# Optimization experiments

Hardware: AMD Instinct MI355X
Metric: run time of the kernel (lower is better)

The kernel has to match this reference:

```python
import jax, jax.numpy as jnp
import numpy as np

NUM_HEADS = 8
DIM_HEAD = 64
EMBED = NUM_HEADS * DIM_HEAD  # 512
B, S, L = 2, 128, 128


def setup_inputs() -> dict:
    key = jax.random.key(0)
    k1, k2 = jax.random.split(key)
    x = jax.random.normal(k1, (B, EMBED, S, L), dtype=jnp.float32)
    # 1x1 Conv2d == pointwise linear over channels: weight [3E, E], bias [3E]
    W = jax.random.normal(k2, (3 * EMBED, EMBED), dtype=jnp.float32) * (EMBED ** -0.5)
    b = jnp.zeros((3 * EMBED,), dtype=jnp.float32)
    return {"x": x, "W": W, "b": b}


def reference(x, W, b):
    Bsz, D, S_, L_ = x.shape
    H, Dh = NUM_HEADS, DIM_HEAD
    scale = Dh ** -0.5
    # QKV projection (1x1 conv)
    qkv = jnp.einsum('oi,bisl->bosl', W, x) + b[None, :, None, None]
    q, k, v = jnp.split(qkv, 3, axis=1)
    q = q.reshape(Bsz, H, Dh, S_, L_) * scale
    k = k.reshape(Bsz, H, Dh, S_, L_)
    v = v.reshape(Bsz, H, Dh, S_, L_)
    # Column attention: attend along S axis, independently per column l
    col_scores = jnp.einsum('bhdsl,bhdtl->bhlst', q, k)      # [B,H,L,S,S]
    col_attn = jax.nn.softmax(col_scores, axis=-1)
    out_col = jnp.einsum('bhlst,bhdtl->bhdsl', col_attn, v)  # [B,H,Dh,S,L]
    # Row attention: attend along L axis, independently per row s
    row_scores = jnp.einsum('bhdsl,bhdsm->bhslm', q, k)      # [B,H,S,L,L]
    row_attn = jax.nn.softmax(row_scores, axis=-1)
    out_row = jnp.einsum('bhslm,bhdsm->bhdsl', row_attn, v)  # [B,H,Dh,S,L]
    out = (out_col + out_row).reshape(Bsz, H * Dh, S_, L_)
    return out
```

## Files before the change

kernel.cpp:

```cpp
#include <hip/hip_runtime.h>
#include <stdint.h>

#define EMB 512
#define THREE_E 1536
#define SL 16384
#define K_DIM 512

typedef unsigned short ushort;
typedef short bf16x8 __attribute__((ext_vector_type(8)));
typedef float f32x4 __attribute__((ext_vector_type(4)));

__device__ __forceinline__ ushort f2bf(float f) {
  unsigned u = __float_as_uint(f);
  u += 0x7fffu + ((u >> 16) & 1u);
  return (ushort)(u >> 16);
}
__device__ __forceinline__ float bf2f(ushort s) {
  return __uint_as_float((unsigned)s << 16);
}

__device__ __forceinline__ void async16(const ushort* g, ushort* l) {
  __builtin_amdgcn_global_load_lds(
      (const __attribute__((address_space(1))) unsigned int*)g,
      (__attribute__((address_space(3))) unsigned int*)l, 16, 0, 0);
}

__global__ __launch_bounds__(256) void wconv(const float* __restrict__ W,
                                             ushort* __restrict__ Wb) {
  int i = blockIdx.x * 256 + threadIdx.x;
  float4 f = ((const float4*)W)[i];
  uint2 o;
  o.x = (unsigned)f2bf(f.x) | ((unsigned)f2bf(f.y) << 16);
  o.y = (unsigned)f2bf(f.z) | ((unsigned)f2bf(f.w) << 16);
  ((uint2*)Wb)[i] = o;
}

__global__ __launch_bounds__(256) void xpose(const float* __restrict__ x,
                                             ushort* __restrict__ xT) {
  __shared__ ushort t[64][65];
  int b = blockIdx.z;
  int i0 = blockIdx.y * 64;
  int n0 = blockIdx.x * 64;
  int c = threadIdx.x & 63;
  int r0 = threadIdx.x >> 6;
  const float* xp = x + ((size_t)(b * EMB + i0)) * SL + n0;
  #pragma unroll
  for (int rr = 0; rr < 16; rr++) {
    int r = r0 * 16 + rr;
    t[r][c] = f2bf(xp[(size_t)r * SL + c]);
  }
  __syncthreads();
  ushort* op = xT + ((size_t)(b * SL + n0)) * EMB + i0;
  #pragma unroll
  for (int rr = 0; rr < 16; rr++) {
    int rn = r0 * 16 + rr;
    op[(size_t)rn * EMB + c] = t[c][rn];
  }
}

__global__ __launch_bounds__(256) void qkv_gemm(const ushort* __restrict__ Wb,
                                                const ushort* __restrict__ xT,
                                                const float* __restrict__ bias,
                                                ushort* __restrict__ rowQ) {
  __shared__ __align__(16) char sm[34816];
  ushort* As = (ushort*)sm;
  ushort* Bs = (ushort*)(sm + 16384);
  const int tid = threadIdx.x;
  const int b = blockIdx.z;
  const int m0 = blockIdx.y * 128;
  const int n0 = blockIdx.x * 128;
  const int lane = tid & 63;
  const int w = tid >> 6;
  const int wr = (w >> 1) * 64;
  const int wc = (w & 1) * 64;
  const int l15 = lane & 15;
  const int quad = lane >> 4;
  const ushort* xb = xT + (size_t)b * SL * EMB;
  f32x4 acc[4][4] = {};
  const int r8 = lane >> 3;
  const int cg = (lane & 7) ^ r8;
  for (int k0 = 0; k0 < K_DIM; k0 += 64) {
    __syncthreads();
    #pragma unroll
    for (int t = 0; t < 4; t++) {
      int seg = 4 * w + t;
      int row = seg * 8 + r8;
      async16(&Wb[(size_t)(m0 + row) * K_DIM + k0 + cg * 8], &As[seg * 512]);
      async16(&xb[(size_t)(n0 + row) * K_DIM + k0 + cg * 8], &Bs[seg * 512]);
    }
    __syncthreads();
    #pragma unroll
    for (int ks = 0; ks < 2; ks++) {
      bf16x8 av[4], bv[4];
      #pragma unroll
      for (int mt = 0; mt < 4; mt++) {
        int row = wr + mt * 16 + l15;
        av[mt] = *(const bf16x8*)&As[row * 64 + (((ks * 4 + quad) ^ (row & 7)) * 8)];
      }
      #pragma unroll
      for (int nt = 0; nt < 4; nt++) {
        int row = wc + nt * 16 + l15;
        bv[nt] = *(const bf16x8*)&Bs[row * 64 + (((ks * 4 + quad) ^ (row & 7)) * 8)];
      }
      #pragma unroll
      for (int mt = 0; mt < 4; mt++)
        #pragma unroll
        for (int nt = 0; nt < 4; nt++)
          acc[mt][nt] = __builtin_amdgcn_mfma_f32_16x16x32_bf16(av[mt], bv[nt], acc[mt][nt], 0, 0, 0);
    }
  }
  __syncthreads();
  {
    ushort* epi = (ushort*)sm;
    const float sc = (m0 < EMB) ? 0.125f : 1.0f;
    const int q4r = quad * 4;
    #pragma unroll
    for (int mt = 0; mt < 4; mt++) {
      int mb = wr + mt * 16 + q4r;
      float b0 = bias[m0 + mb], b1 = bias[m0 + mb + 1];
      float b2 = bias[m0 + mb + 2], b3 = bias[m0 + mb + 3];
      #pragma unroll
      for (int nt = 0; nt < 4; nt++) {
        int l = wc + nt * 16 + l15;
        unsigned u0 = f2bf((acc[mt][nt][0] + b0) * sc);
        unsigned u1 = f2bf((acc[mt][nt][1] + b1) * sc);
        unsigned u2 = f2bf((acc[mt][nt][2] + b2) * sc);
        unsigned u3 = f2bf((acc[mt][nt][3] + b3) * sc);
        uint2 pk;
        pk.x = u0 | (u1 << 16);
        pk.y = u2 | (u3 << 16);
        *(uint2*)&epi[l * 136 + mb] = pk;
      }
    }
  }
  __syncthreads();
  {
    const ushort* epi = (const ushort*)sm;
    const int sel = m0 >> 9;
    const int hb = (m0 & 511) >> 6;
    const int s = blockIdx.x;
    #pragma unroll
    for (int it = 0; it < 8; it++) {
      int flat = it * 2048 + tid * 8;
      int head = flat >> 13;
      int rem = flat & 8191;
      int l = rem >> 6;
      int dd = rem & 63;
      size_t dst = ((((size_t)(b * 3 + sel) * 8 + hb + head) * 128 + s) * 128 + l) * 64 + dd;
      *(uint4*)&rowQ[dst] = *(const uint4*)&epi[l * 136 + head * 64 + dd];
    }
  }
}

template <int COL>
__global__ __launch_bounds__(256) void attn3(const ushort* __restrict__ qkv,
                                             ushort* __restrict__ tmp,
                                             float* __restrict__ out) {
  __shared__ ushort Ks[128 * 64];
  __shared__ ushort Vt[64 * 136];
  __shared__ ushort Ps[64 * 136];
  const int tid = threadIdx.x;
  const int fixed = blockIdx.x;
  const int h = blockIdx.y, b = blockIdx.z;
  const int w = tid >> 6, lane = tid & 63, l15 = lane & 15, quad = lane >> 4;
  const size_t off = COL ? (size_t)fixed * 64 : (size_t)fixed * 8192;
  const size_t tstr = COL ? 8192 : 64;
  const ushort* Qg = qkv + ((size_t)(b * 3 + 0) * 8 + h) * 1048576 + off;
  const ushort* Kg = Qg + (size_t)8 * 1048576;
  const ushort* Vg = Qg + (size_t)16 * 1048576;
  ushort* tb = tmp + (size_t)(b * 8 + h) * 1048576;
  {
    int r8k = lane >> 3;
    int cgk = (lane & 7) ^ r8k;
    #pragma unroll
    for (int t = 0; t < 4; t++) {
      int seg = 4 * w + t;
      int row = seg * 8 + r8k;
      async16(&Kg[(size_t)row * tstr + cgk * 8], &Ks[seg * 512]);
    }
  }
  {
    int trow = tid >> 3, d0 = (tid & 7) * 8, dg = tid & 7;
    #pragma unroll
    for (int it = 0; it < 4; it++) {
      int t = trow + it * 32;
      uint4 vv = *(const uint4*)&Vg[(size_t)t * tstr + d0];
      ushort* vs = (ushort*)&vv;
      #pragma unroll
      for (int k = 0; k < 8; k++) {
        int i = (k + dg) & 7;
        Vt[(d0 + i) * 136 + t] = vs[i];
      }
    }
  }
  bf16x8 aq[2][2];
  #pragma unroll
  for (int c = 0; c < 2; c++) {
    const ushort* qp = Qg + (size_t)(c * 64 + w * 16 + l15) * tstr + quad * 8;
    aq[c][0] = *(const bf16x8*)qp;
    aq[c][1] = *(const bf16x8*)(qp + 32);
  }
  uint2 treg[2][4];
  if (!COL) {
    #pragma unroll
    for (int c = 0; c < 2; c++) {
      const ushort* tp = tb + (size_t)(c * 64 + w * 16 + l15) * 8192 + (size_t)fixed * 64 + quad * 4;
      #pragma unroll
      for (int mt = 0; mt < 4; mt++) treg[c][mt] = *(const uint2*)(tp + mt * 16);
    }
  }
  __syncthreads();
  const int rx = l15 & 7;
  #pragma unroll
  for (int c = 0; c < 2; c++) {
    f32x4 accS[8];
    #pragma unroll
    for (int nt = 0; nt < 8; nt++) {
      int row = nt * 16 + l15;
      bf16x8 bk0 = *(const bf16x8*)&Ks[row * 64 + ((quad ^ rx) * 8)];
      bf16x8 bk1 = *(const bf16x8*)&Ks[row * 64 + (((quad + 4) ^ rx) * 8)];
      f32x4 z = {0.f, 0.f, 0.f, 0.f};
      z = __builtin_amdgcn_mfma_f32_16x16x32_bf16(aq[c][0], bk0, z, 0, 0, 0);
      z = __builtin_amdgcn_mfma_f32_16x16x32_bf16(aq[c][1], bk1, z, 0, 0, 0);
      accS[nt] = z;
    }
    float inv[4];
    #pragma unroll
    for (int r = 0; r < 4; r++) {
      float mx = accS[0][r];
      #pragma unroll
      for (int nt = 1; nt < 8; nt++) mx = fmaxf(mx, accS[nt][r]);
      mx = fmaxf(mx, __shfl_xor(mx, 1));
      mx = fmaxf(mx, __shfl_xor(mx, 2));
      mx = fmaxf(mx, __shfl_xor(mx, 4));
      mx = fmaxf(mx, __shfl_xor(mx, 8));
      float s = 0.f;
      #pragma unroll
      for (int nt = 0; nt < 8; nt++) {
        float p = __builtin_amdgcn_exp2f((accS[nt][r] - mx) * 1.44269504088896f);
        accS[nt][r] = p;
        s += p;
      }
      s += __shfl_xor(s, 1);
      s += __shfl_xor(s, 2);
      s += __shfl_xor(s, 4);
      s += __shfl_xor(s, 8);
      inv[r] = 1.0f / s;
    }
    asm volatile("s_waitcnt lgkmcnt(0)" ::: "memory");
    #pragma unroll
    for (int nt = 0; nt < 8; nt++)
      #pragma unroll
      for (int r = 0; r < 4; r++)
        Ps[(w * 16 + quad * 4 + r) * 136 + nt * 16 + l15] = f2bf(accS[nt][r] * inv[r]);
    asm volatile("s_waitcnt lgkmcnt(0)" ::: "memory");
    f32x4 accO[4] = {{0.f,0.f,0.f,0.f},{0.f,0.f,0.f,0.f},{0.f,0.f,0.f,0.f},{0.f,0.f,0.f,0.f}};
    #pragma unroll
    for (int kf = 0; kf < 4; kf++) {
      bf16x8 p = *(const bf16x8*)&Ps[(w * 16 + l15) * 136 + kf * 32 + quad * 8];
      #pragma unroll
      for (int t4 = 0; t4 < 4; t4++) {
        bf16x8 v = *(const bf16x8*)&Vt[(t4 * 16 + l15) * 136 + kf * 32 + quad * 8];
        accO[t4] = COL ? __builtin_amdgcn_mfma_f32_16x16x32_bf16(p, v, accO[t4], 0, 0, 0)
                       : __builtin_amdgcn_mfma_f32_16x16x32_bf16(v, p, accO[t4], 0, 0, 0);
      }
    }
    if (COL) {
      ushort* tp = tb + (size_t)fixed * 8192 + c * 4096;
      #pragma unroll
      for (int t4 = 0; t4 < 4; t4++)
        #pragma unroll
        for (int r = 0; r < 4; r++)
          tp[(w * 16 + quad * 4 + r) * 64 + t4 * 16 + l15] = f2bf(accO[t4][r]);
    } else {
      float* ob = out + (size_t)(b * EMB + h * 64) * SL + (size_t)fixed * 128 + c * 64 + w * 16 + l15;
      #pragma unroll
      for (int t4 = 0; t4 < 4; t4++) {
        const ushort* tr = (const ushort*)&treg[c][t4];
        #pragma unroll
        for (int r = 0; r < 4; r++)
          ob[(size_t)(t4 * 16 + quad * 4 + r) * SL] = accO[t4][r] + bf2f(tr[r]);
      }
    }
  }
}

extern "C" void kernel_launch(void* const* d_in, const int* in_sizes, int n_in,
                              void* d_out, int out_size, void* d_ws, size_t ws_size,
                              hipStream_t stream) {
  const float* x = (const float*)d_in[0];
  const float* W = (const float*)d_in[1];
  const float* bias = (const float*)d_in[2];
  float* out = (float*)d_out;
  ushort* rowQ = (ushort*)d_ws;
  ushort* xT = (ushort*)((char*)d_ws + 100663296);
  ushort* tmp = (ushort*)((char*)d_ws + 100663296);
  ushort* Wb = (ushort*)((char*)d_ws + 134217728);

  hipLaunchKernelGGL(wconv, dim3(768), dim3(256), 0, stream, W, Wb);
  hipLaunchKernelGGL(xpose, dim3(256, 8, 2), dim3(256), 0, stream, x, xT);
  hipLaunchKernelGGL(qkv_gemm, dim3(128, 12, 2), dim3(256), 0, stream, Wb, xT, bias, rowQ);
  hipLaunchKernelGGL(attn3<1>, dim3(128, 8, 2), dim3(256), 0, stream, rowQ, tmp, out);
  hipLaunchKernelGGL(attn3<0>, dim3(128, 8, 2), dim3(256), 0, stream, rowQ, tmp, out);
}
```

Before: 259.5 us.

## Rewrite QKV GEMM as 256x256 tiles with double-buffered async LDS pipeline

The QKV projection GEMM moves from 128x128 tiles with 4 waves and a single LDS buffer to 256x256 tiles with 8 waves and double-buffered 128KB shared memory. Global-to-LDS async loads for the next K slice are interleaved with MFMA phases using explicit vmcnt/lgkmcnt waits, barriers and s_setprio. The aim is to hide load latency and raise arithmetic intensity per block. The epilogue now stages per-wave tiles to write the row-layout output. The cost is much larger LDS use, fewer blocks (768 instead of 3072) and fragile hand-tuned synchronisation.

```diff
diff --git a/kernel.cpp b/kernel.cpp
--- a/kernel.cpp
+++ b/kernel.cpp
@@ -58,98 +58,154 @@
   }
 }
 
-__global__ __launch_bounds__(256) void qkv_gemm(const ushort* __restrict__ Wb,
-                                                const ushort* __restrict__ xT,
-                                                const float* __restrict__ bias,
-                                                ushort* __restrict__ rowQ) {
-  __shared__ __align__(16) char sm[34816];
-  ushort* As = (ushort*)sm;
-  ushort* Bs = (ushort*)(sm + 16384);
+__global__ __launch_bounds__(512, 2) void qkv_gemm(const ushort* __restrict__ Wb,
+                                                   const ushort* __restrict__ xT,
+                                                   const float* __restrict__ bias,
+                                                   ushort* __restrict__ rowQ) {
+  __shared__ __align__(16) char sm[131072];
+  ushort* const A0 = (ushort*)sm;
+  ushort* const B0 = (ushort*)(sm + 32768);
+  ushort* const A1 = (ushort*)(sm + 65536);
+  ushort* const B1 = (ushort*)(sm + 98304);
   const int tid = threadIdx.x;
-  const int b = blockIdx.z;
-  const int m0 = blockIdx.y * 128;
-  const int n0 = blockIdx.x * 128;
-  const int lane = tid & 63;
-  const int w = tid >> 6;
-  const int wr = (w >> 1) * 64;
-  const int wc = (w & 1) * 64;
-  const int l15 = lane & 15;
-  const int quad = lane >> 4;
-  const ushort* xb = xT + (size_t)b * SL * EMB;
-  f32x4 acc[4][4] = {};
+  const int bz = blockIdx.z;
+  const int m0 = blockIdx.y * 256;
+  const int n0 = blockIdx.x * 256;
+  const int lane = tid & 63, w = tid >> 6;
+  const int wm = w >> 2, wn = w & 3;
+  const int l15 = lane & 15, quad = lane >> 4;
   const int r8 = lane >> 3;
-  const int cg = (lane & 7) ^ r8;
-  for (int k0 = 0; k0 < K_DIM; k0 += 64) {
-    __syncthreads();
-    #pragma unroll
-    for (int t = 0; t < 4; t++) {
-      int seg = 4 * w + t;
-      int row = seg * 8 + r8;
-      async16(&Wb[(size_t)(m0 + row) * K_DIM + k0 + cg * 8], &As[seg * 512]);
-      async16(&xb[(size_t)(n0 + row) * K_DIM + k0 + cg * 8], &Bs[seg * 512]);
-    }
-    __syncthreads();
-    #pragma unroll
-    for (int ks = 0; ks < 2; ks++) {
-      bf16x8 av[4], bv[4];
-      #pragma unroll
-      for (int mt = 0; mt < 4; mt++) {
-        int row = wr + mt * 16 + l15;
-        av[mt] = *(const bf16x8*)&As[row * 64 + (((ks * 4 + quad) ^ (row & 7)) * 8)];
-      }
-      #pragma unroll
-      for (int nt = 0; nt < 4; nt++) {
-        int row = wc + nt * 16 + l15;
-        bv[nt] = *(const bf16x8*)&Bs[row * 64 + (((ks * 4 + quad) ^ (row & 7)) * 8)];
-      }
-      #pragma unroll
-      for (int mt = 0; mt < 4; mt++)
-        #pragma unroll
-        for (int nt = 0; nt < 4; nt++)
-          acc[mt][nt] = __builtin_amdgcn_mfma_f32_16x16x32_bf16(av[mt], bv[nt], acc[mt][nt], 0, 0, 0);
-    }
-  }
+  const int cg8 = ((lane & 7) ^ r8) * 8;
+  const int rx = l15 & 7;
+  const ushort* Wt = Wb + (size_t)m0 * K_DIM;
+  const ushort* Xt = xT + ((size_t)bz * SL + n0) * K_DIM;
+
+  f32x4 acc[8][4] = {};
+  bf16x8 av[4][2], bv0[2][2], bv1[2][2];
+
+#define STG(gb, lb)                                                       \
+  async16((gb) + (size_t)(w * 8 + r8) * K_DIM + cg8, (lb) + w * 512);     \
+  async16((gb) + (size_t)(w * 8 + r8 + 64) * K_DIM + cg8, (lb) + w * 512 + 4096)
+
+#define LDA(AP, MH)                                                           \
+  _Pragma("unroll") for (int mt = 0; mt < 4; mt++) {                          \
+    const int row = wm * 128 + (MH) * 64 + mt * 16 + l15;                     \
+    av[mt][0] = *(const bf16x8*)&(AP)[row * 64 + ((quad ^ rx) * 8)];          \
+    av[mt][1] = *(const bf16x8*)&(AP)[row * 64 + (((quad + 4) ^ rx) * 8)];    \
+  }
+
+#define LDB(BP, NH, BV)                                                       \
+  _Pragma("unroll") for (int nt = 0; nt < 2; nt++) {                          \
+    const int row = wn * 64 + (NH) * 32 + nt * 16 + l15;                      \
+    BV[nt][0] = *(const bf16x8*)&(BP)[row * 64 + ((quad ^ rx) * 8)];          \
+    BV[nt][1] = *(const bf16x8*)&(BP)[row * 64 + (((quad + 4) ^ rx) * 8)];    \
+  }
+
+#define MM(MH, NH, BV)                                                        \
+  __builtin_amdgcn_s_setprio(1);                                              \
+  _Pragma("unroll") for (int mt = 0; mt < 4; mt++)                            \
+  _Pragma("unroll") for (int nt = 0; nt < 2; nt++) {                          \
+    acc[(MH) * 4 + mt][(NH) * 2 + nt] =                                       \
+        __builtin_amdgcn_mfma_f32_16x16x32_bf16(                              \
+            av[mt][0], BV[nt][0], acc[(MH) * 4 + mt][(NH) * 2 + nt], 0, 0, 0);\
+    acc[(MH) * 4 + mt][(NH) * 2 + nt] =                                       \
+        __builtin_amdgcn_mfma_f32_16x16x32_bf16(                              \
+            av[mt][1], BV[nt][1], acc[(MH) * 4 + mt][(NH) * 2 + nt], 0, 0, 0);\
+  }                                                                           \
+  __builtin_amdgcn_s_setprio(0)
+
+#define BAR __builtin_amdgcn_s_barrier()
+#define LGKM0 asm volatile("s_waitcnt lgkmcnt(0)" ::: "memory")
+#define VMC(N) asm volatile("s_waitcnt vmcnt(" #N ")" ::: "memory")
+
+  STG(Xt, B0);
+  STG(Xt + 65536, B0 + 8192);
+  STG(Wt, A0);
+  STG(Wt + 65536, A0 + 8192);
+  STG(Xt + 64, B1);
+  STG(Xt + 65536 + 64, B1 + 8192);
+  VMC(4);
+  BAR;
+
+  for (int t = 0; t < 4; ++t) {
+    const int kB = t * 128 + 64;
+    const int kN = t * 128 + 128;
+    const int kN2 = t * 128 + 192;
+    const bool st = (t < 3);
+    LDA(A0, 0); LDB(B0, 0, bv0);
+    STG(Wt + kB, A1);
+    BAR; LGKM0; MM(0, 0, bv0); BAR;
+    LDB(B0, 1, bv1);
+    STG(Wt + 65536 + kB, A1 + 8192);
+    BAR; LGKM0; MM(0, 1, bv1); BAR;
+    LDA(A0, 1);
+    if (st) { STG(Xt + kN, B0); }
+    BAR; LGKM0; MM(1, 1, bv1); BAR;
+    if (st) { STG(Xt + 65536 + kN, B0 + 8192); }
+    BAR; MM(1, 0, bv0);
+    if (t == 3) { VMC(0); } else { VMC(4); }
+    BAR;
+    LDA(A1, 0); LDB(B1, 0, bv0);
+    if (st) { STG(Wt + kN, A0); }
+    BAR; LGKM0; MM(0, 0, bv0); BAR;
+    LDB(B1, 1, bv1);
+    if (st) { STG(Wt + 65536 + kN, A0 + 8192); }
+    BAR; LGKM0; MM(0, 1, bv1); BAR;
+    LDA(A1, 1);
+    if (st) { STG(Xt + kN2, B1); }
+    BAR; LGKM0; MM(1, 1, bv1); BAR;
+    if (st) { STG(Xt + 65536 + kN2, B1 + 8192); }
+    BAR; MM(1, 0, bv0);
+    if (st) { VMC(4); }
+    BAR;
+  }
+
   __syncthreads();
   {
-    ushort* epi = (ushort*)sm;
-    const float sc = (m0 < EMB) ? 0.125f : 1.0f;
-    const int q4r = quad * 4;
-    #pragma unroll
-    for (int mt = 0; mt < 4; mt++) {
-      int mb = wr + mt * 16 + q4r;
-      float b0 = bias[m0 + mb], b1 = bias[m0 + mb + 1];
-      float b2 = bias[m0 + mb + 2], b3 = bias[m0 + mb + 3];
-      #pragma unroll
-      for (int nt = 0; nt < 4; nt++) {
-        int l = wc + nt * 16 + l15;
-        unsigned u0 = f2bf((acc[mt][nt][0] + b0) * sc);
-        unsigned u1 = f2bf((acc[mt][nt][1] + b1) * sc);
-        unsigned u2 = f2bf((acc[mt][nt][2] + b2) * sc);
-        unsigned u3 = f2bf((acc[mt][nt][3] + b3) * sc);
-        uint2 pk;
-        pk.x = u0 | (u1 << 16);
-        pk.y = u2 | (u3 << 16);
-        *(uint2*)&epi[l * 136 + mb] = pk;
-      }
-    }
-  }
-  __syncthreads();
-  {
-    const ushort* epi = (const ushort*)sm;
-    const int sel = m0 >> 9;
-    const int hb = (m0 & 511) >> 6;
-    const int s = blockIdx.x;
-    #pragma unroll
-    for (int it = 0; it < 8; it++) {
-      int flat = it * 2048 + tid * 8;
-      int head = flat >> 13;
-      int rem = flat & 8191;
-      int l = rem >> 6;
-      int dd = rem & 63;
-      size_t dst = ((((size_t)(b * 3 + sel) * 8 + hb + head) * 128 + s) * 128 + l) * 64 + dd;
-      *(uint4*)&rowQ[dst] = *(const uint4*)&epi[l * 136 + head * 64 + dd];
-    }
-  }
+    ushort* ep = (ushort*)sm + w * 4608;
+    const float sc = (m0 < 512) ? 0.125f : 1.0f;
+    const int q4 = quad * 4;
+    const int sidx = (n0 >> 7) + (wn >> 1);
+    const int lbase = (wn & 1) * 64;
+    const int ml = (lane & 7) * 8;
+    const int nlo = lane >> 3;
+    #pragma unroll
+    for (int mh = 0; mh < 2; ++mh) {
+      if (mh) { LGKM0; }
+      #pragma unroll
+      for (int mt = 0; mt < 4; ++mt) {
+        const int mloc = mt * 16 + q4;
+        const int mg = m0 + wm * 128 + mh * 64 + mloc;
+        const float b0 = bias[mg], b1 = bias[mg + 1];
+        const float b2 = bias[mg + 2], b3 = bias[mg + 3];
+        #pragma unroll
+        for (int nt = 0; nt < 4; ++nt) {
+          const f32x4 a = acc[mh * 4 + mt][nt];
+          uint2 pk;
+          pk.x = (unsigned)f2bf((a[0] + b0) * sc) | ((unsigned)f2bf((a[1] + b1) * sc) << 16);
+          pk.y = (unsigned)f2bf((a[2] + b2) * sc) | ((unsigned)f2bf((a[3] + b3) * sc) << 16);
+          *(uint2*)&ep[(nt * 16 + l15) * 72 + mloc] = pk;
+        }
+      }
+      LGKM0;
+      const int mb0 = m0 + wm * 128 + mh * 64;
+      const int sel = mb0 >> 9;
+      const int hh = (mb0 >> 6) & 7;
+      ushort* db = rowQ + ((((size_t)(bz * 3 + sel) * 8 + hh) * 128 + sidx) * 128) * 64;
+      #pragma unroll
+      for (int it = 0; it < 8; ++it) {
+        const int nl = it * 8 + nlo;
+        *(uint4*)&db[(size_t)(lbase + nl) * 64 + ml] = *(const uint4*)&ep[nl * 72 + ml];
+      }
+    }
+  }
+#undef STG
+#undef LDA
+#undef LDB
+#undef MM
+#undef BAR
+#undef LGKM0
+#undef VMC
 }
 
 template <int COL>
@@ -299,7 +355,7 @@
 
   hipLaunchKernelGGL(wconv, dim3(768), dim3(256), 0, stream, W, Wb);
   hipLaunchKernelGGL(xpose, dim3(256, 8, 2), dim3(256), 0, stream, x, xT);
-  hipLaunchKernelGGL(qkv_gemm, dim3(128, 12, 2), dim3(256), 0, stream, Wb, xT, bias, rowQ);
+  hipLaunchKernelGGL(qkv_gemm, dim3(64, 6, 2), dim3(512), 0, stream, Wb, xT, bias, rowQ);
   hipLaunchKernelGGL(attn3<1>, dim3(128, 8, 2), dim3(256), 0, stream, rowQ, tmp, out);
   hipLaunchKernelGGL(attn3<0>, dim3(128, 8, 2), dim3(256), 0, stream, rowQ, tmp, out);
 }
```

Measured after the change: 256.1 us. No clear change (-1.3%).

## Double-buffer QKV GEMM K-loop, vectorize transpose, reorder grid for W reuse

Applied to the files above, without the earlier changes.

The QKV GEMM now double-buffers LDS tiles with 32-wide K stages, issuing async global-to-LDS loads for the next stage while MFMAs run on the current one. It uses explicit vmcnt/lgkmcnt waits, raw barriers and s_setprio around the MFMA block, and sets a 3-blocks-per-CU launch bound. The grid is swapped so the M-blocks (weight rows) vary fastest, letting the blocks that share an xT tile run close together. The transpose kernel is also rewritten to use float4 loads and 8-byte stores, at the cost of more complex swizzle indexing and hand-tuned wait counts that must stay correct.

```diff
diff --git a/kernel.cpp b/kernel.cpp
--- a/kernel.cpp
+++ b/kernel.cpp
@@ -37,78 +37,129 @@
 
 __global__ __launch_bounds__(256) void xpose(const float* __restrict__ x,
                                              ushort* __restrict__ xT) {
-  __shared__ ushort t[64][65];
+  __shared__ ushort t[64][68];
   int b = blockIdx.z;
   int i0 = blockIdx.y * 64;
   int n0 = blockIdx.x * 64;
-  int c = threadIdx.x & 63;
-  int r0 = threadIdx.x >> 6;
+  int tid = threadIdx.x;
   const float* xp = x + ((size_t)(b * EMB + i0)) * SL + n0;
   #pragma unroll
-  for (int rr = 0; rr < 16; rr++) {
-    int r = r0 * 16 + rr;
-    t[r][c] = f2bf(xp[(size_t)r * SL + c]);
+  for (int it = 0; it < 4; it++) {
+    int f = it * 256 + tid;
+    int r = f >> 4, c4 = (f & 15) * 4;
+    float4 v = *(const float4*)&xp[(size_t)r * SL + c4];
+    uint2 p;
+    p.x = (unsigned)f2bf(v.x) | ((unsigned)f2bf(v.y) << 16);
+    p.y = (unsigned)f2bf(v.z) | ((unsigned)f2bf(v.w) << 16);
+    *(uint2*)&t[r][c4] = p;
   }
   __syncthreads();
   ushort* op = xT + ((size_t)(b * SL + n0)) * EMB + i0;
   #pragma unroll
-  for (int rr = 0; rr < 16; rr++) {
-    int rn = r0 * 16 + rr;
-    op[(size_t)rn * EMB + c] = t[c][rn];
-  }
-}
-
-__global__ __launch_bounds__(256) void qkv_gemm(const ushort* __restrict__ Wb,
-                                                const ushort* __restrict__ xT,
-                                                const float* __restrict__ bias,
-                                                ushort* __restrict__ rowQ) {
+  for (int it = 0; it < 4; it++) {
+    int u = it * 256 + tid;
+    int n = u >> 4, i4 = (u & 15) * 4;
+    uint2 p;
+    ushort* ps = (ushort*)&p;
+    #pragma unroll
+    for (int j = 0; j < 4; j++) ps[j] = t[i4 + j][n];
+    *(uint2*)&op[(size_t)n * EMB + i4] = p;
+  }
+}
+
+__global__ __launch_bounds__(256, 3) void qkv_gemm(const ushort* __restrict__ Wb,
+                                                   const ushort* __restrict__ xT,
+                                                   const float* __restrict__ bias,
+                                                   ushort* __restrict__ rowQ) {
   __shared__ __align__(16) char sm[34816];
-  ushort* As = (ushort*)sm;
-  ushort* Bs = (ushort*)(sm + 16384);
+  ushort* const A0 = (ushort*)sm;
+  ushort* const B0 = (ushort*)(sm + 8192);
+  ushort* const A1 = (ushort*)(sm + 16384);
+  ushort* const B1 = (ushort*)(sm + 24576);
   const int tid = threadIdx.x;
   const int b = blockIdx.z;
-  const int m0 = blockIdx.y * 128;
-  const int n0 = blockIdx.x * 128;
+  const int m0 = blockIdx.x * 128;
+  const int n0 = blockIdx.y * 128;
   const int lane = tid & 63;
   const int w = tid >> 6;
   const int wr = (w >> 1) * 64;
   const int wc = (w & 1) * 64;
   const int l15 = lane & 15;
   const int quad = lane >> 4;
-  const ushort* xb = xT + (size_t)b * SL * EMB;
+  const int hn = l15 & 1;
+  const int r0s = w * 8 + (lane >> 3);
+  const int cs = lane & 7;
+  const ushort* Ag = Wb + (size_t)m0 * K_DIM;
+  const ushort* Bg = xT + ((size_t)b * SL + n0) * K_DIM;
   f32x4 acc[4][4] = {};
-  const int r8 = lane >> 3;
-  const int cg = (lane & 7) ^ r8;
-  for (int k0 = 0; k0 < K_DIM; k0 += 64) {
-    __syncthreads();
-    #pragma unroll
-    for (int t = 0; t < 4; t++) {
-      int seg = 4 * w + t;
-      int row = seg * 8 + r8;
-      async16(&Wb[(size_t)(m0 + row) * K_DIM + k0 + cg * 8], &As[seg * 512]);
-      async16(&xb[(size_t)(n0 + row) * K_DIM + k0 + cg * 8], &Bs[seg * 512]);
-    }
-    __syncthreads();
-    #pragma unroll
-    for (int ks = 0; ks < 2; ks++) {
+
+#define STG32(gb, lb)                                                     \
+  {                                                                       \
+    _Pragma("unroll") for (int j = 0; j < 2; j++) {                       \
+      int row = j * 32 + r0s;                                             \
+      int q = cs ^ (row & 7);                                             \
+      int n = 2 * row + (q >> 2);                                         \
+      async16((gb) + (size_t)n * K_DIM + (q & 3) * 8,                     \
+              (lb) + j * 2048 + w * 512);                                 \
+    }                                                                     \
+  }
+
+#define FRAGS(AP, BP)                                                     \
+  _Pragma("unroll") for (int mt = 0; mt < 4; mt++) {                      \
+    int n = wr + mt * 16 + l15;                                           \
+    int R = n >> 1;                                                       \
+    av[mt] = *(const bf16x8*)&(AP)[R * 64 + (((quad | (hn << 2)) ^ (R & 7)) * 8)]; \
+  }                                                                       \
+  _Pragma("unroll") for (int nt = 0; nt < 4; nt++) {                      \
+    int n = wc + nt * 16 + l15;                                           \
+    int R = n >> 1;                                                       \
+    bv[nt] = *(const bf16x8*)&(BP)[R * 64 + (((quad | (hn << 2)) ^ (R & 7)) * 8)]; \
+  }
+
+#define MFMA16                                                            \
+  __builtin_amdgcn_s_setprio(1);                                          \
+  _Pragma("unroll") for (int mt = 0; mt < 4; mt++)                        \
+  _Pragma("unroll") for (int nt = 0; nt < 4; nt++)                        \
+    acc[mt][nt] = __builtin_amdgcn_mfma_f32_16x16x32_bf16(av[mt], bv[nt], acc[mt][nt], 0, 0, 0); \
+  __builtin_amdgcn_s_setprio(0)
+
+#define BAR __builtin_amdgcn_s_barrier()
+#define LGKM0 asm volatile("s_waitcnt lgkmcnt(0)" ::: "memory")
+#define VMC(N) asm volatile("s_waitcnt vmcnt(" #N ")" ::: "memory")
+
+  STG32(Ag, A0);
+  STG32(Bg, B0);
+
+  #pragma unroll
+  for (int tp = 0; tp < 8; ++tp) {
+    {
+      STG32(Ag + (2 * tp + 1) * 32, A1);
+      STG32(Bg + (2 * tp + 1) * 32, B1);
+      VMC(4);
+      BAR;
       bf16x8 av[4], bv[4];
-      #pragma unroll
-      for (int mt = 0; mt < 4; mt++) {
-        int row = wr + mt * 16 + l15;
-        av[mt] = *(const bf16x8*)&As[row * 64 + (((ks * 4 + quad) ^ (row & 7)) * 8)];
-      }
-      #pragma unroll
-      for (int nt = 0; nt < 4; nt++) {
-        int row = wc + nt * 16 + l15;
-        bv[nt] = *(const bf16x8*)&Bs[row * 64 + (((ks * 4 + quad) ^ (row & 7)) * 8)];
-      }
-      #pragma unroll
-      for (int mt = 0; mt < 4; mt++)
-        #pragma unroll
-        for (int nt = 0; nt < 4; nt++)
-          acc[mt][nt] = __builtin_amdgcn_mfma_f32_16x16x32_bf16(av[mt], bv[nt], acc[mt][nt], 0, 0, 0);
-    }
-  }
+      FRAGS(A0, B0);
+      LGKM0;
+      MFMA16;
+      BAR;
+    }
+    {
+      if (tp < 7) {
+        STG32(Ag + (2 * tp + 2) * 32, A0);
+        STG32(Bg + (2 * tp + 2) * 32, B0);
+        VMC(4);
+      } else {
+        VMC(0);
+      }
+      BAR;
+      bf16x8 av[4], bv[4];
+      FRAGS(A1, B1);
+      LGKM0;
+      MFMA16;
+      BAR;
+    }
+  }
+
   __syncthreads();
   {
     ushort* epi = (ushort*)sm;
@@ -138,7 +189,7 @@
     const ushort* epi = (const ushort*)sm;
     const int sel = m0 >> 9;
     const int hb = (m0 & 511) >> 6;
-    const int s = blockIdx.x;
+    const int s = blockIdx.y;
     #pragma unroll
     for (int it = 0; it < 8; it++) {
       int flat = it * 2048 + tid * 8;
@@ -150,6 +201,12 @@
       *(uint4*)&rowQ[dst] = *(const uint4*)&epi[l * 136 + head * 64 + dd];
     }
   }
+#undef STG32
+#undef FRAGS
+#undef MFMA16
+#undef BAR
+#undef LGKM0
+#undef VMC
 }
 
 template <int COL>
@@ -299,7 +356,7 @@
 
   hipLaunchKernelGGL(wconv, dim3(768), dim3(256), 0, stream, W, Wb);
   hipLaunchKernelGGL(xpose, dim3(256, 8, 2), dim3(256), 0, stream, x, xT);
-  hipLaunchKernelGGL(qkv_gemm, dim3(128, 12, 2), dim3(256), 0, stream, Wb, xT, bias, rowQ);
+  hipLaunchKernelGGL(qkv_gemm, dim3(12, 128, 2), dim3(256), 0, stream, Wb, xT, bias, rowQ);
   hipLaunchKernelGGL(attn3<1>, dim3(128, 8, 2), dim3(256), 0, stream, rowQ, tmp, out);
   hipLaunchKernelGGL(attn3<0>, dim3(128, 8, 2), dim3(256), 0, stream, rowQ, tmp, out);
 }
```

Result: no change. 257.9 us (-0.6%).

## Load GEMM fragments directly from global, remap blocks per XCD, vectorize transpose

Applied to the files above, without the earlier changes.

The QKV GEMM stops staging tiles through LDS with barriers. Each wave now loads its MFMA fragments straight from global memory into registers, double-buffered across 16 k-steps, with setprio raised around the MFMA burst. The grid is flattened to 1D and remapped so that all 12 M-tiles of an N-panel land on the same XCD, sharing its L2. The transpose kernel now uses float4 loads and packed uint2 stores. The tradeoff is that fragments are re-read from global/L2 by multiple waves with uncoalesced 16-byte per-lane accesses, and register pressure rises.

```diff
diff --git a/kernel.cpp b/kernel.cpp
--- a/kernel.cpp
+++ b/kernel.cpp
@@ -37,78 +37,92 @@
 
 __global__ __launch_bounds__(256) void xpose(const float* __restrict__ x,
                                              ushort* __restrict__ xT) {
-  __shared__ ushort t[64][65];
+  __shared__ ushort t[64][68];
   int b = blockIdx.z;
   int i0 = blockIdx.y * 64;
   int n0 = blockIdx.x * 64;
-  int c = threadIdx.x & 63;
-  int r0 = threadIdx.x >> 6;
+  int tid = threadIdx.x;
   const float* xp = x + ((size_t)(b * EMB + i0)) * SL + n0;
   #pragma unroll
-  for (int rr = 0; rr < 16; rr++) {
-    int r = r0 * 16 + rr;
-    t[r][c] = f2bf(xp[(size_t)r * SL + c]);
+  for (int it = 0; it < 4; it++) {
+    int f = it * 256 + tid;
+    int r = f >> 4, c4 = (f & 15) * 4;
+    float4 v = *(const float4*)&xp[(size_t)r * SL + c4];
+    uint2 p;
+    p.x = (unsigned)f2bf(v.x) | ((unsigned)f2bf(v.y) << 16);
+    p.y = (unsigned)f2bf(v.z) | ((unsigned)f2bf(v.w) << 16);
+    *(uint2*)&t[r][c4] = p;
   }
   __syncthreads();
   ushort* op = xT + ((size_t)(b * SL + n0)) * EMB + i0;
   #pragma unroll
-  for (int rr = 0; rr < 16; rr++) {
-    int rn = r0 * 16 + rr;
-    op[(size_t)rn * EMB + c] = t[c][rn];
-  }
-}
-
-__global__ __launch_bounds__(256) void qkv_gemm(const ushort* __restrict__ Wb,
-                                                const ushort* __restrict__ xT,
-                                                const float* __restrict__ bias,
-                                                ushort* __restrict__ rowQ) {
+  for (int it = 0; it < 4; it++) {
+    int u = it * 256 + tid;
+    int n = u >> 4, i4 = (u & 15) * 4;
+    uint2 p;
+    ushort* ps = (ushort*)&p;
+    #pragma unroll
+    for (int j = 0; j < 4; j++) ps[j] = t[i4 + j][n];
+    *(uint2*)&op[(size_t)n * EMB + i4] = p;
+  }
+}
+
+__global__ __launch_bounds__(256, 3) void qkv_gemm(const ushort* __restrict__ Wb,
+                                                   const ushort* __restrict__ xT,
+                                                   const float* __restrict__ bias,
+                                                   ushort* __restrict__ rowQ) {
   __shared__ __align__(16) char sm[34816];
-  ushort* As = (ushort*)sm;
-  ushort* Bs = (ushort*)(sm + 16384);
   const int tid = threadIdx.x;
-  const int b = blockIdx.z;
-  const int m0 = blockIdx.y * 128;
-  const int n0 = blockIdx.x * 128;
+  const int wg = blockIdx.x;
+  const int xcd = wg & 7;
+  const int q = wg >> 3;
+  const int b = q / 192;
+  const int r = q - b * 192;
+  const int npan = (r / 12) * 8 + xcd;
+  const int m = r % 12;
+  const int m0 = m * 128;
+  const int n0 = npan * 128;
   const int lane = tid & 63;
   const int w = tid >> 6;
   const int wr = (w >> 1) * 64;
   const int wc = (w & 1) * 64;
   const int l15 = lane & 15;
   const int quad = lane >> 4;
-  const ushort* xb = xT + (size_t)b * SL * EMB;
+  const ushort* ap[4];
+  const ushort* bp[4];
+  #pragma unroll
+  for (int mt = 0; mt < 4; mt++)
+    ap[mt] = Wb + (size_t)(m0 + wr + mt * 16 + l15) * K_DIM + quad * 8;
+  #pragma unroll
+  for (int nt = 0; nt < 4; nt++)
+    bp[nt] = xT + ((size_t)b * SL + n0 + wc + nt * 16 + l15) * K_DIM + quad * 8;
+
   f32x4 acc[4][4] = {};
-  const int r8 = lane >> 3;
-  const int cg = (lane & 7) ^ r8;
-  for (int k0 = 0; k0 < K_DIM; k0 += 64) {
-    __syncthreads();
-    #pragma unroll
-    for (int t = 0; t < 4; t++) {
-      int seg = 4 * w + t;
-      int row = seg * 8 + r8;
-      async16(&Wb[(size_t)(m0 + row) * K_DIM + k0 + cg * 8], &As[seg * 512]);
-      async16(&xb[(size_t)(n0 + row) * K_DIM + k0 + cg * 8], &Bs[seg * 512]);
-    }
-    __syncthreads();
-    #pragma unroll
-    for (int ks = 0; ks < 2; ks++) {
-      bf16x8 av[4], bv[4];
-      #pragma unroll
-      for (int mt = 0; mt < 4; mt++) {
-        int row = wr + mt * 16 + l15;
-        av[mt] = *(const bf16x8*)&As[row * 64 + (((ks * 4 + quad) ^ (row & 7)) * 8)];
-      }
-      #pragma unroll
-      for (int nt = 0; nt < 4; nt++) {
-        int row = wc + nt * 16 + l15;
-        bv[nt] = *(const bf16x8*)&Bs[row * 64 + (((ks * 4 + quad) ^ (row & 7)) * 8)];
-      }
-      #pragma unroll
-      for (int mt = 0; mt < 4; mt++)
-        #pragma unroll
-        for (int nt = 0; nt < 4; nt++)
-          acc[mt][nt] = __builtin_amdgcn_mfma_f32_16x16x32_bf16(av[mt], bv[nt], acc[mt][nt], 0, 0, 0);
-    }
-  }
+  bf16x8 af[2][4], bf[2][4];
+  #pragma unroll
+  for (int mt = 0; mt < 4; mt++) af[0][mt] = *(const bf16x8*)(ap[mt]);
+  #pragma unroll
+  for (int nt = 0; nt < 4; nt++) bf[0][nt] = *(const bf16x8*)(bp[nt]);
+
+  #pragma unroll
+  for (int s = 0; s < 16; s++) {
+    const int cur = s & 1, nxt = cur ^ 1;
+    if (s < 15) {
+      #pragma unroll
+      for (int mt = 0; mt < 4; mt++) af[nxt][mt] = *(const bf16x8*)(ap[mt] + (s + 1) * 32);
+      #pragma unroll
+      for (int nt = 0; nt < 4; nt++) bf[nxt][nt] = *(const bf16x8*)(bp[nt] + (s + 1) * 32);
+    }
+    __builtin_amdgcn_s_setprio(1);
+    #pragma unroll
+    for (int mt = 0; mt < 4; mt++)
+      #pragma unroll
+      for (int nt = 0; nt < 4; nt++)
+        acc[mt][nt] = __builtin_amdgcn_mfma_f32_16x16x32_bf16(af[cur][mt], bf[cur][nt],
+                                                              acc[mt][nt], 0, 0, 0);
+    __builtin_amdgcn_s_setprio(0);
+  }
+
   __syncthreads();
   {
     ushort* epi = (ushort*)sm;
@@ -138,7 +152,7 @@
     const ushort* epi = (const ushort*)sm;
     const int sel = m0 >> 9;
     const int hb = (m0 & 511) >> 6;
-    const int s = blockIdx.x;
+    const int s = n0 >> 7;
     #pragma unroll
     for (int it = 0; it < 8; it++) {
       int flat = it * 2048 + tid * 8;
@@ -299,7 +313,7 @@
 
   hipLaunchKernelGGL(wconv, dim3(768), dim3(256), 0, stream, W, Wb);
   hipLaunchKernelGGL(xpose, dim3(256, 8, 2), dim3(256), 0, stream, x, xT);
-  hipLaunchKernelGGL(qkv_gemm, dim3(128, 12, 2), dim3(256), 0, stream, Wb, xT, bias, rowQ);
+  hipLaunchKernelGGL(qkv_gemm, dim3(3072), dim3(256), 0, stream, Wb, xT, bias, rowQ);
   hipLaunchKernelGGL(attn3<1>, dim3(128, 8, 2), dim3(256), 0, stream, rowQ, tmp, out);
   hipLaunchKernelGGL(attn3<0>, dim3(128, 8, 2), dim3(256), 0, stream, rowQ, tmp, out);
 }
```

Result: slower. 366.7 us (+41.3%).
